# Performance work log

Measured on AMD Instinct MI355X. Metric: run time of the kernel, lower is better.

The kernel has to match this reference:

```python
import jax, jax.numpy as jnp
import numpy as np
from itertools import combinations, product

NQ = 10
DIM = 2 ** NQ
DEPTH = 1
ENC_PAIRS = [(q, q + 1) for q in range(0, NQ - 1, 2)] + [(q, q + 1) for q in range(1, NQ - 1, 2)]  # brick layer: even then odd
PYR = [(i, i + 1) for layer in range(NQ - 1) for i in range(NQ - layer - 1)]  # pyramid RBS wire pairs (45)
OBS_PAIRS = list(combinations(range(NQ), 2))  # 45 pairwise 2-local observables

_P = {'I': np.eye(2, dtype=np.complex128),
      'X': np.array([[0, 1], [1, 0]], dtype=np.complex128),
      'Y': np.array([[0, -1j], [1j, 0]], dtype=np.complex128),
      'Z': np.array([[1, 0], [0, -1]], dtype=np.complex128)}
_WORDS = [''.join(w) for w in product('IXYZ', repeat=2)][1:]  # PennyLane pauli_basis order, identity excluded
P15 = jnp.asarray(np.stack([np.kron(_P[w[0]], _P[w[1]]) for w in _WORDS]).astype(np.complex64))
XXm = jnp.asarray(np.kron(_P['X'], _P['X']).astype(np.complex64))
YYm = jnp.asarray(np.kron(_P['Y'], _P['Y']).astype(np.complex64))
ZZm = jnp.asarray(np.kron(_P['Z'], _P['Z']).astype(np.complex64))
I4 = jnp.eye(4, dtype=jnp.complex64)
_TRIL_I, _TRIL_J = np.tril_indices(4, -1)  # order matches create_Hermitian's count+j indexing


def _u3(t, p, l):
    c = jnp.cos(t / 2).astype(jnp.complex64)
    s = jnp.sin(t / 2).astype(jnp.complex64)
    return jnp.stack([jnp.stack([c, -jnp.exp(1j * l) * s]),
                      jnp.stack([jnp.exp(1j * p) * s, jnp.exp(1j * (p + l)) * c])])


def _ising(phi, P):
    # exp(-i*phi/2 * P) for P in {XX, YY, ZZ} (P^2 = I)
    return jnp.cos(phi / 2) * I4 - 1j * jnp.sin(phi / 2) * P


def _apply1(psi, U, w):
    # psi: (B, 2, ..., 2); single-qubit gate U (2,2) on wire w
    psi = jnp.moveaxis(psi, 1 + w, -1)
    sh = psi.shape
    out = jnp.einsum('ij,brj->bri', U, psi.reshape(sh[0], -1, 2)).reshape(sh)
    return jnp.moveaxis(out, -1, 1 + w)


def _apply2(psi, U, a, b):
    # two-qubit gate on wires (a,b), a is most-significant (PennyLane wire order). U: (4,4) or batched (B,4,4)
    psi = jnp.moveaxis(psi, (1 + a, 1 + b), (-2, -1))
    sh = psi.shape
    flat = psi.reshape(sh[0], -1, 4)
    eq = 'bij,brj->bri' if U.ndim == 3 else 'ij,brj->bri'
    out = jnp.einsum(eq, U, flat).reshape(sh)
    return jnp.moveaxis(out, (-2, -1), (1 + a, 1 + b))


def _build_H(A, B, D):
    # create_Hermitian: lower triangle A+iB, diag[0:3] = D[1:4], diag[3]=0, then h + h^dagger
    n = A.shape[0]
    h = jnp.zeros((n, 4, 4), jnp.complex64)
    h = h.at[:, _TRIL_I, _TRIL_J].set(A.astype(jnp.complex64) + 1j * B.astype(jnp.complex64))
    d = np.arange(3)
    h = h.at[:, d, d].set(D[:, 1:4].astype(jnp.complex64))
    return h + jnp.conj(jnp.swapaxes(h, -1, -2))


def setup_inputs() -> dict:
    key = jax.random.key(0)
    ks = jax.random.split(key, 9)
    f32 = jnp.float32
    return {
        'x': jax.random.normal(ks[0], (256, 512), f32),
        'W1': jax.random.normal(ks[1], (512, 256), f32) * (512 ** -0.5),
        'b1': jnp.zeros((256,), f32),
        'W2': jax.random.normal(ks[2], (256, 135), f32) * (256 ** -0.5),
        'b2': jnp.zeros((135,), f32),
        'qvit_params': 0.01 * jax.random.normal(ks[3], (DEPTH, len(PYR), 12), f32),
        'A': 2.0 * jax.random.normal(ks[4], (len(OBS_PAIRS), 6), f32),
        'B': 2.0 * jax.random.normal(ks[5], (len(OBS_PAIRS), 6), f32),
        'D': 2.0 * jax.random.normal(ks[6], (len(OBS_PAIRS), 4), f32),
    }


def reference(x, W1, b1, W2, b2, qvit_params, A, B, D):
    Bsz = x.shape[0]
    # enc_proj: Linear -> SiLU -> Linear
    enc = jax.nn.silu(x @ W1 + b1) @ W2 + b2  # (B, 135)
    # Brick-layer SpecialUnitary encoding: U = exp(i * sum theta_m P_m) via eigh
    theta = enc.reshape(Bsz, len(ENC_PAIRS), 15).astype(jnp.complex64)
    Hg = jnp.einsum('bgm,mij->bgij', theta, P15)  # Hermitian generators (B, 9, 4, 4)
    ew, V = jnp.linalg.eigh(Hg)
    Ue = jnp.einsum('bgik,bgk,bgjk->bgij', V, jnp.exp(1j * ew.astype(jnp.complex64)), jnp.conj(V))
    # |0...0>
    psi = jnp.zeros((Bsz, DIM), jnp.complex64).at[:, 0].set(1.0).reshape((Bsz,) + (2,) * NQ)
    for g, (a, b) in enumerate(ENC_PAIRS):
        psi = _apply2(psi, Ue[:, g], a, b)
    # QViT pyramid ansatz
    for ly in range(DEPTH):
        for g, (a, b) in enumerate(PYR):
            p = qvit_params[ly, g]
            psi = _apply1(psi, _u3(p[0], p[1], p[2]), a)
            psi = _apply2(psi, _ising(p[3], XXm), a, b)
            psi = _apply2(psi, _ising(p[4], YYm), a, b)
            psi = _apply2(psi, _ising(p[5], ZZm), a, b)
            psi = _apply1(psi, _u3(p[6], p[7], p[8]), a)
            psi = _apply2(psi, _ising(p[9], XXm), a, b)
            psi = _apply2(psi, _ising(p[10], YYm), a, b)
            psi = _apply2(psi, _ising(p[11], ZZm), a, b)
    # Pairwise ANO Hermitian expectations
    Hobs = _build_H(A, B, D)  # (45, 4, 4)
    outs = []
    for w, (a, b) in enumerate(OBS_PAIRS):
        pm = jnp.moveaxis(psi, (1 + a, 1 + b), (1, 2)).reshape(Bsz, 4, -1)
        outs.append(jnp.real(jnp.einsum('bir,ij,bjr->b', jnp.conj(pm), Hobs[w], pm)))
    return jnp.stack(outs, axis=1).astype(jnp.float32)
```

## Files before the change

### kernel.cpp

```cpp
#include <hip/hip_runtime.h>
#include <math.h>

#define NOBS 45
typedef float2 c32;

__device__ __constant__ int PA_s[NOBS] = {
    1,1,1,1,1,1,1,1,1, 0,0,0,0,0,0,0,0, 7,7,7,7,7,7,7, 6,6,6,6,6,6,
    5,5,5,5,5, 3,3,3,3, 2,2,2, 4,4, 9};
__device__ __constant__ int PB_s[NOBS] = {
    0,7,6,5,3,2,4,9,8, 7,6,5,3,2,4,9,8, 6,5,3,2,4,9,8, 5,3,2,4,9,8,
    3,2,4,9,8, 2,4,9,8, 4,9,8, 9,8, 8};
constexpr int TIc[6] = {1, 2, 2, 3, 3, 3};
constexpr int TJc[6] = {0, 0, 1, 0, 1, 2};

__device__ __forceinline__ c32 cfma(c32 a, c32 b, c32 c) {
    c.x = fmaf(a.x, b.x, fmaf(-a.y, b.y, c.x));
    c.y = fmaf(a.x, b.y, fmaf(a.y, b.x, c.y));
    return c;
}
__device__ __forceinline__ c32 cmul(c32 a, c32 b) {
    return make_float2(a.x * b.x - a.y * b.y, a.x * b.y + a.y * b.x);
}

template <int CTRL>
__device__ __forceinline__ float dppf(float x) {
    return __uint_as_float((unsigned)__builtin_amdgcn_update_dpp(
        0, (int)__float_as_uint(x), CTRL, 0xF, 0xF, true));
}
__device__ __forceinline__ float swap32f(float a) {
    auto r = __builtin_amdgcn_permlane32_swap(__float_as_uint(a), __float_as_uint(a), false, false);
    return (__uint_as_float(r[0]) + __uint_as_float(r[1])) - a;
}
#if __has_builtin(__builtin_amdgcn_permlane16_swap)
__device__ __forceinline__ float swap16f(float a) {
    auto r = __builtin_amdgcn_permlane16_swap(__float_as_uint(a), __float_as_uint(a), false, false);
    return (__uint_as_float(r[0]) + __uint_as_float(r[1])) - a;
}
#else
__device__ __forceinline__ float swap16f(float a) { return __shfl_xor(a, 16, 64); }
#endif
__device__ __forceinline__ float swz4f(float a) {
    return __uint_as_float(__builtin_amdgcn_ds_swizzle(__float_as_uint(a), 0x101F));
}
template <int M>
__device__ __forceinline__ float exf(float x) {
    float r = x;
    if constexpr ((M & 3) == 1) r = dppf<0xB1>(r);
    else if constexpr ((M & 3) == 2) r = dppf<0x4E>(r);
    else if constexpr ((M & 3) == 3) r = dppf<0x1B>(r);
    if constexpr (M & 4)  r = swz4f(r);
    if constexpr (M & 8)  r = dppf<0x128>(r);
    if constexpr (M & 16) r = swap16f(r);
    if constexpr (M & 32) r = swap32f(r);
    return r;
}
template <int M>
__device__ __forceinline__ c32 exch(c32 a) { return make_float2(exf<M>(a.x), exf<M>(a.y)); }
__device__ __forceinline__ c32 swap32c(c32 a) { return make_float2(swap32f(a.x), swap32f(a.y)); }

__device__ __forceinline__ float wave_reduce63(float x) {
    x += dppf<0x111>(x);
    x += dppf<0x112>(x);
    x += dppf<0x114>(x);
    x += dppf<0x118>(x);
    x += dppf<0x142>(x);
    x += dppf<0x143>(x);
    return x;
}

__device__ __forceinline__ int insert2(int t, int pl, int ph) {
    int low  = t & ((1 << pl) - 1);
    int rest = t >> pl;
    int nm   = ph - 1 - pl;
    int mid  = rest & ((1 << nm) - 1);
    int high = rest >> nm;
    return low | (mid << (pl + 1)) | (high << (ph + 1));
}

template <int W>
__device__ __forceinline__ c32 pE(int r, int c) {
    if constexpr (W == 0) return make_float2((r == c) ? 1.f : 0.f, 0.f);
    else if constexpr (W == 1) return make_float2((r != c) ? 1.f : 0.f, 0.f);
    else if constexpr (W == 2) return make_float2(0.f, (r == c) ? 0.f : ((r == 0) ? -1.f : 1.f));
    else return make_float2((r == c) ? ((r == 0) ? 1.f : -1.f) : 0.f, 0.f);
}
template <int W0, int W1>
__device__ __forceinline__ void paccum(c32& H, float th, int i1, int i2, int j1, int j2) {
    c32 a = pE<W0>(i1, j1), b = pE<W1>(i2, j2);
    c32 p = cmul(a, b);
    H.x = fmaf(th, p.x, H.x);
    H.y = fmaf(th, p.y, H.y);
}

struct F16 { c32 u[16]; };
struct FLoc { c32 a[4]; c32 b[4]; };
struct F4 { c32 uS, uB, uA, uC; };

__device__ __forceinline__ F16 loadF16(const c32* __restrict__ U) {
    F16 f;
#pragma unroll
    for (int i = 0; i < 16; i++) f.u[i] = U[i];
    return f;
}
__device__ __forceinline__ FLoc loadLoc(const c32* __restrict__ U, int ln) {
    int bb = (ln >> 5) & 1;
    const c32* U0 = U + bb * 4;
    const c32* U1 = U + (2 | bb) * 4;
    int c00 = bb, c01 = 2 | bb, c10 = bb ^ 1, c11 = 2 | (bb ^ 1);
    FLoc f;
    f.a[0] = U0[c00]; f.a[1] = U0[c01]; f.a[2] = U0[c10]; f.a[3] = U0[c11];
    f.b[0] = U1[c00]; f.b[1] = U1[c01]; f.b[2] = U1[c10]; f.b[3] = U1[c11];
    return f;
}
template <int QA, int QB>
__device__ __forceinline__ F4 loadL2(const c32* __restrict__ U, int ln) {
    int bA = (ln >> QA) & 1, bB = (ln >> QB) & 1;
    int r = (bA << 1) | bB;
    const c32* Ur = U + r * 4;
    F4 f;
    f.uS = Ur[r]; f.uB = Ur[r ^ 1]; f.uA = Ur[r ^ 2]; f.uC = Ur[r ^ 3];
    return f;
}

__device__ __forceinline__ void applyLL(c32 v[4], const F16& f) {
    c32 n0 = cfma(f.u[0],  v[0], cfma(f.u[1],  v[1], cfma(f.u[2],  v[2], cmul(f.u[3],  v[3]))));
    c32 n1 = cfma(f.u[4],  v[0], cfma(f.u[5],  v[1], cfma(f.u[6],  v[2], cmul(f.u[7],  v[3]))));
    c32 n2 = cfma(f.u[8],  v[0], cfma(f.u[9],  v[1], cfma(f.u[10], v[2], cmul(f.u[11], v[3]))));
    c32 n3 = cfma(f.u[12], v[0], cfma(f.u[13], v[1], cfma(f.u[14], v[2], cmul(f.u[15], v[3]))));
    v[0] = n0; v[1] = n1; v[2] = n2; v[3] = n3;
}
__device__ __forceinline__ void applyLoc(c32 v[4], const FLoc& f) {
    c32 p0 = swap32c(v[0]), p1 = swap32c(v[1]), p2 = swap32c(v[2]), p3 = swap32c(v[3]);
    c32 n0 = cfma(f.a[0], v[0], cfma(f.a[1], v[1], cfma(f.a[2], p0, cmul(f.a[3], p1))));
    c32 n1 = cfma(f.b[0], v[0], cfma(f.b[1], v[1], cfma(f.b[2], p0, cmul(f.b[3], p1))));
    c32 n2 = cfma(f.a[0], v[2], cfma(f.a[1], v[3], cfma(f.a[2], p2, cmul(f.a[3], p3))));
    c32 n3 = cfma(f.b[0], v[2], cfma(f.b[1], v[3], cfma(f.b[2], p2, cmul(f.b[3], p3))));
    v[0] = n0; v[1] = n1; v[2] = n2; v[3] = n3;
}
template <int QA, int QB>
__device__ __forceinline__ void applyL2(c32 v[4], const F4& f) {
#pragma unroll
    for (int lc = 0; lc < 4; lc++) {
        c32 pB = exch<(1 << QB)>(v[lc]);
        c32 pA = exch<(1 << QA)>(v[lc]);
        c32 pC = exch<(1 << QA)>(pB);
        v[lc] = cfma(f.uS, v[lc], cfma(f.uB, pB, cfma(f.uA, pA, cmul(f.uC, pC))));
    }
}

__device__ __forceinline__ void dumpV(const c32 v[4], c32* __restrict__ psi, int t) {
#pragma unroll
    for (int lc = 0; lc < 4; lc++) psi[(t << 2) | lc] = v[lc];
}
__device__ __forceinline__ void loadV(c32 v[4], const c32* __restrict__ psi, int t) {
#pragma unroll
    for (int lc = 0; lc < 4; lc++) v[lc] = psi[(t << 2) | lc];
}
template <int PA, int PB>
__device__ __forceinline__ void ldsApply(const F16& f, c32* __restrict__ psi, int t) {
    constexpr int PL = (PA < PB) ? PA : PB, PH = (PA < PB) ? PB : PA;
    int base = insert2(t, PL, PH);
    constexpr int oa = 1 << PA, ob = 1 << PB;
    c32 g0 = psi[base], g1 = psi[base + ob], g2 = psi[base + oa], g3 = psi[base + oa + ob];
    c32 n0 = cfma(f.u[0],  g0, cfma(f.u[1],  g1, cfma(f.u[2],  g2, cmul(f.u[3],  g3))));
    c32 n1 = cfma(f.u[4],  g0, cfma(f.u[5],  g1, cfma(f.u[6],  g2, cmul(f.u[7],  g3))));
    c32 n2 = cfma(f.u[8],  g0, cfma(f.u[9],  g1, cfma(f.u[10], g2, cmul(f.u[11], g3))));
    c32 n3 = cfma(f.u[12], g0, cfma(f.u[13], g1, cfma(f.u[14], g2, cmul(f.u[15], g3))));
    psi[base] = n0; psi[base + ob] = n1; psi[base + oa] = n2; psi[base + oa + ob] = n3;
}

__global__ __launch_bounds__(256, 1) void mega_kernel(
    const float* __restrict__ x,  const float* __restrict__ W1, const float* __restrict__ b1,
    const float* __restrict__ W2, const float* __restrict__ b2, const float* __restrict__ qp,
    const float* __restrict__ Am, const float* __restrict__ Bm, const float* __restrict__ Dm,
    float* __restrict__ out) {
    __shared__ __align__(16) c32 psiS[1024];
    __shared__ c32 UeS[144];
    __shared__ c32 GpS[720];
    __shared__ float HbS[720];
    __shared__ float encS[136];
    __shared__ float redS[180];

    const int b = blockIdx.x, t = threadIdx.x, ln = t & 63;
    float* F = (float*)psiS;

    if (t < 128) ((float4*)F)[t] = ((const float4*)(x + (size_t)b * 512))[t];
    __syncthreads();
    {
        int q = t & 63, sl = t >> 6;
        float4 a4 = make_float4(0.f, 0.f, 0.f, 0.f);
#pragma unroll 16
        for (int kk = 0; kk < 128; kk++) {
            int k = sl * 128 + kk;
            float xk = F[k];
            const float4 w = *(const float4*)(W1 + (size_t)k * 256 + q * 4);
            a4.x = fmaf(xk, w.x, a4.x); a4.y = fmaf(xk, w.y, a4.y);
            a4.z = fmaf(xk, w.z, a4.z); a4.w = fmaf(xk, w.w, a4.w);
        }
        *(float4*)(F + 512 + sl * 256 + q * 4) = a4;
    }
    __syncthreads();
    {
        float hv = b1[t] + F[512 + t] + F[768 + t] + F[1024 + t] + F[1280 + t];
        hv = hv / (1.f + __expf(-hv));
        F[1536 + t] = hv;
    }
    __syncthreads();
    if (t < 135) {
        float a2 = b2[t], a3 = 0.f;
#pragma unroll 16
        for (int k = 0; k < 128; k++) {
            a2 = fmaf(F[1536 + k],       W2[(size_t)k * 135 + t],         a2);
            a3 = fmaf(F[1536 + 128 + k], W2[(size_t)(128 + k) * 135 + t], a3);
        }
        encS[t] = a2 + a3;
    }
    __syncthreads();

    c32* Mm = psiS;
    c32* Rb = psiS + 144;
    c32* TA = psiS + 288;
    if (t < 144) {
        int m = t >> 4, e = t & 15, i = e >> 2, j = e & 3;
        int i1 = i >> 1, i2 = i & 1, j1 = j >> 1, j2 = j & 1;
        const float* th = encS + m * 15;
        c32 H = make_float2(0.f, 0.f);
        paccum<0,1>(H, th[0],  i1,i2,j1,j2); paccum<0,2>(H, th[1],  i1,i2,j1,j2);
        paccum<0,3>(H, th[2],  i1,i2,j1,j2); paccum<1,0>(H, th[3],  i1,i2,j1,j2);
        paccum<1,1>(H, th[4],  i1,i2,j1,j2); paccum<1,2>(H, th[5],  i1,i2,j1,j2);
        paccum<1,3>(H, th[6],  i1,i2,j1,j2); paccum<2,0>(H, th[7],  i1,i2,j1,j2);
        paccum<2,1>(H, th[8],  i1,i2,j1,j2); paccum<2,2>(H, th[9],  i1,i2,j1,j2);
        paccum<2,3>(H, th[10], i1,i2,j1,j2); paccum<3,0>(H, th[11], i1,i2,j1,j2);
        paccum<3,1>(H, th[12], i1,i2,j1,j2); paccum<3,2>(H, th[13], i1,i2,j1,j2);
        paccum<3,3>(H, th[14], i1,i2,j1,j2);
        const float sc = 1.f / 64.f;
        Mm[t] = make_float2(-H.y * sc, H.x * sc);
        Rb[t] = make_float2((i == j) ? 1.f : 0.f, 0.f);
    } else if (t >= 234) {
        for (int w = t - 234; w < NOBS; w += 22) {
            float* Hf = HbS + w * 16;
            Hf[0] = 2.f * Dm[w * 4 + 1];
            Hf[1] = 2.f * Dm[w * 4 + 2];
            Hf[2] = 2.f * Dm[w * 4 + 3];
            Hf[3] = 0.f;
#pragma unroll
            for (int k = 0; k < 6; k++) {
                Hf[4 + 2 * k] = 2.f * Am[w * 6 + k];
                Hf[5 + 2 * k] = 2.f * Bm[w * 6 + k];
            }
        }
    }
    __syncthreads();
    c32 Mrow[4];
    if (t < 144) {
        int m = t >> 4, i = (t & 15) >> 2;
#pragma unroll
        for (int k = 0; k < 4; k++) Mrow[k] = Mm[m * 16 + i * 4 + k];
    }
#pragma unroll 1
    for (int step = 0; step < 13; step++) {
        if (t < 144) {
            int m = t >> 4, e = t & 15, i = e >> 2, j = e & 3;
            const c32* cur = (step & 1) ? UeS : Rb;
            c32 acc = make_float2(0.f, 0.f);
            c32 outv;
            if (step < 7) {
#pragma unroll
                for (int k = 0; k < 4; k++) acc = cfma(Mrow[k], cur[m * 16 + k * 4 + j], acc);
                float inv = 1.f / (float)(7 - step);
                outv = make_float2(fmaf(acc.x, inv, (i == j) ? 1.f : 0.f), acc.y * inv);
            } else {
#pragma unroll
                for (int k = 0; k < 4; k++)
                    acc = cfma(cur[m * 16 + i * 4 + k], cur[m * 16 + k * 4 + j], acc);
                outv = acc;
            }
            ((step & 1) ? Rb : UeS)[t] = outv;
        } else if (t >= 144 && t < 234 && step < 8) {
            int pt = t - 144, g = pt >> 1, ih = (pt & 1) << 1;
            const float* p = qp + g * 12;
            const c32* src = ((step & 1) ? TA : GpS) + g * 16;
            c32* dst = ((step & 1) ? GpS : TA) + g * 16;
#pragma unroll
            for (int r2 = 0; r2 < 2; r2++) {
                int i = ih + r2, i1 = i >> 1, i2 = i & 1;
                c32 row[4];
                if (step == 0) {
                    float s, c; __sincosf(p[0] * 0.5f, &s, &c);
                    c32 u0, u1;
                    if (i1 == 0) { u0 = make_float2(c, 0.f);
                                   u1 = make_float2(-__cosf(p[2]) * s, -__sinf(p[2]) * s); }
                    else { u0 = make_float2(__cosf(p[1]) * s, __sinf(p[1]) * s);
                           u1 = make_float2(__cosf(p[1] + p[2]) * c, __sinf(p[1] + p[2]) * c); }
#pragma unroll
                    for (int jj = 0; jj < 4; jj++) row[jj] = make_float2(0.f, 0.f);
                    row[i2] = u0; row[2 | i2] = u1;
                } else {
                    c32 coef0, coef1; int c0, c1;
                    if (step == 1 || step == 5) {
                        float s, c; __sincosf(p[step == 1 ? 3 : 9] * 0.5f, &s, &c);
                        c0 = i; coef0 = make_float2(c, 0.f);
                        c1 = i ^ 3; coef1 = make_float2(0.f, -s);
                    } else if (step == 2 || step == 6) {
                        float s, c; __sincosf(p[step == 2 ? 4 : 10] * 0.5f, &s, &c);
                        float yy = (i == 0 || i == 3) ? 1.f : -1.f;
                        c0 = i; coef0 = make_float2(c, 0.f);
                        c1 = i ^ 3; coef1 = make_float2(0.f, s * yy);
                    } else if (step == 3 || step == 7) {
                        float s, c; __sincosf(p[step == 3 ? 5 : 11] * 0.5f, &s, &c);
                        float zz = (i == 0 || i == 3) ? 1.f : -1.f;
                        c0 = i; coef0 = make_float2(c, -s * zz);
                        c1 = i; coef1 = make_float2(0.f, 0.f);
                    } else {
                        float s, c; __sincosf(p[6] * 0.5f, &s, &c);
                        if (i1 == 0) { coef0 = make_float2(c, 0.f);
                                       coef1 = make_float2(-__cosf(p[8]) * s, -__sinf(p[8]) * s); }
                        else { coef0 = make_float2(__cosf(p[7]) * s, __sinf(p[7]) * s);
                               coef1 = make_float2(__cosf(p[7] + p[8]) * c, __sinf(p[7] + p[8]) * c); }
                        c0 = i2; c1 = 2 | i2;
                    }
#pragma unroll
                    for (int jj = 0; jj < 4; jj++)
                        row[jj] = cfma(coef0, src[c0 * 4 + jj], cmul(coef1, src[c1 * 4 + jj]));
                }
#pragma unroll
                for (int jj = 0; jj < 4; jj++) dst[i * 4 + jj] = row[jj];
            }
        }
        __syncthreads();
    }

    c32 v[4];
#pragma unroll
    for (int lc = 0; lc < 4; lc++) v[lc] = make_float2(0.f, 0.f);
    if (t == 0) v[0] = make_float2(1.f, 0.f);

    applyLL(v, loadF16(UeS + 0));
    applyL2<5, 4>(v, loadL2<5, 4>(UeS + 16, ln));
    applyL2<3, 1>(v, loadL2<3, 1>(UeS + 32, ln));
    applyL2<0, 2>(v, loadL2<0, 2>(UeS + 48, ln));
    dumpV(v, psiS, t); __syncthreads();
    ldsApply<9, 8>(loadF16(UeS + 64), psiS, t); __syncthreads();
    loadV(v, psiS, t);
    applyLoc(v, loadLoc(UeS + 80, ln));
    applyL2<4, 3>(v, loadL2<4, 3>(UeS + 96, ln));
    applyL2<1, 0>(v, loadL2<1, 0>(UeS + 112, ln));
    dumpV(v, psiS, t); __syncthreads();
    ldsApply<4, 9>(loadF16(UeS + 128), psiS, t); __syncthreads();
    loadV(v, psiS, t);

    {
        int g = 0;
#pragma unroll 1
        for (int layer = 0; layer < 9; layer++) {
            const int amax = 8 - layer;
            applyLL(v, loadF16(GpS + (g++) * 16));
            if (amax >= 1) applyLoc(v, loadLoc(GpS + (g++) * 16, ln));
            if (amax >= 2) applyL2<5, 4>(v, loadL2<5, 4>(GpS + (g++) * 16, ln));
            if (amax >= 3) applyL2<4, 3>(v, loadL2<4, 3>(GpS + (g++) * 16, ln));
            if (amax >= 4) applyL2<3, 1>(v, loadL2<3, 1>(GpS + (g++) * 16, ln));
            if (amax >= 5) applyL2<1, 0>(v, loadL2<1, 0>(GpS + (g++) * 16, ln));
            if (amax >= 6) applyL2<0, 2>(v, loadL2<0, 2>(GpS + (g++) * 16, ln));
            if (amax >= 7) {
                dumpV(v, psiS, t); __syncthreads();
                ldsApply<4, 9>(loadF16(GpS + (g++) * 16), psiS, t); __syncthreads();
                if (amax >= 8) {
                    ldsApply<9, 8>(loadF16(GpS + (g++) * 16), psiS, t); __syncthreads();
                }
                loadV(v, psiS, t);
            }
        }
    }

    dumpV(v, psiS, t);
    __syncthreads();
#pragma unroll 1
    for (int w0 = 0; w0 < NOBS; w0 += 5) {
        float pr[5];
#pragma unroll
        for (int u = 0; u < 5; u++) {
            const int w = w0 + u;
            const int pa = PA_s[w], pb = PB_s[w];
            const int pl = (pa < pb) ? pa : pb, phh = (pa < pb) ? pb : pa;
            const int oa = 1 << pa, ob = 1 << pb;
            int i0 = insert2(t, pl, phh);
            c32 vg[4];
            vg[0] = psiS[i0];      vg[1] = psiS[i0 + ob];
            vg[2] = psiS[i0 + oa]; vg[3] = psiS[i0 + oa + ob];
            const float* Hf = HbS + w * 16;
            float r = Hf[0] * fmaf(vg[0].x, vg[0].x, vg[0].y * vg[0].y)
                    + Hf[1] * fmaf(vg[1].x, vg[1].x, vg[1].y * vg[1].y)
                    + Hf[2] * fmaf(vg[2].x, vg[2].x, vg[2].y * vg[2].y);
#pragma unroll
            for (int k = 0; k < 6; k++) {
                c32 vi = vg[TIc[k]], vj = vg[TJc[k]];
                float cx = fmaf(vi.x, vj.x, vi.y * vj.y);
                float cy = fmaf(vi.x, vj.y, -vi.y * vj.x);
                r = fmaf(Hf[4 + 2 * k], cx, r);
                r = fmaf(-Hf[5 + 2 * k], cy, r);
            }
            pr[u] = wave_reduce63(r);
        }
        if (ln == 63) {
#pragma unroll
            for (int u = 0; u < 5; u++) redS[(w0 + u) * 4 + (t >> 6)] = pr[u];
        }
    }
    __syncthreads();
    if (t < NOBS)
        out[(size_t)b * NOBS + t] = redS[t * 4] + redS[t * 4 + 1] + redS[t * 4 + 2] + redS[t * 4 + 3];
}

extern "C" void kernel_launch(void* const* d_in, const int* in_sizes, int n_in,
                              void* d_out, int out_size, void* d_ws, size_t ws_size,
                              hipStream_t stream) {
    (void)in_sizes; (void)n_in; (void)out_size; (void)d_ws; (void)ws_size;
    const float* x  = (const float*)d_in[0];
    const float* W1 = (const float*)d_in[1];
    const float* b1 = (const float*)d_in[2];
    const float* W2 = (const float*)d_in[3];
    const float* b2 = (const float*)d_in[4];
    const float* qp = (const float*)d_in[5];
    const float* Am = (const float*)d_in[6];
    const float* Bm = (const float*)d_in[7];
    const float* Dm = (const float*)d_in[8];
    float* out = (float*)d_out;

    hipLaunchKernelGGL(mega_kernel, dim3(256), dim3(256), 0, stream,
                       x, W1, b1, W2, b2, qp, Am, Bm, Dm, out);
}
```

Before: 112.2 us.

## Double threads per block and remap qubits to halve per-thread state

Doubles the block to 512 threads, so each thread holds 2 amplitudes instead of 4. The qubit-to-bit mapping becomes natural order: one qubit sits in the register index, low qubits in the lane, and qubits 6-9 go through shared memory. Shared-memory gates now use ping-pong buffers, with each thread computing two output rows. The encoder MLP, the observable reduction and the gate loops are repartitioned across 8 waves, and the loops are fully unrolled. The aim is more wave-level parallelism and shorter per-thread dependency chains. The cost is more barriers and cross-lane exchanges, plus each 4x4 gate row being loaded separately per half-block.

```diff
diff --git a/kernel.cpp b/kernel.cpp
--- a/kernel.cpp
+++ b/kernel.cpp
@@ -4,14 +4,12 @@
 #define NOBS 45
 typedef float2 c32;
 
-__device__ __constant__ int PA_s[NOBS] = {
-    1,1,1,1,1,1,1,1,1, 0,0,0,0,0,0,0,0, 7,7,7,7,7,7,7, 6,6,6,6,6,6,
-    5,5,5,5,5, 3,3,3,3, 2,2,2, 4,4, 9};
-__device__ __constant__ int PB_s[NOBS] = {
-    0,7,6,5,3,2,4,9,8, 7,6,5,3,2,4,9,8, 6,5,3,2,4,9,8, 5,3,2,4,9,8,
-    3,2,4,9,8, 2,4,9,8, 4,9,8, 9,8, 8};
-constexpr int TIc[6] = {1, 2, 2, 3, 3, 3};
-constexpr int TJc[6] = {0, 0, 1, 0, 1, 2};
+constexpr int OAc[NOBS] = {
+    0,0,0,0,0,0,0,0,0, 1,1,1,1,1,1,1,1, 2,2,2,2,2,2,2, 3,3,3,3,3,3,
+    4,4,4,4,4, 5,5,5,5, 6,6,6, 7,7, 8};
+constexpr int OBc[NOBS] = {
+    1,2,3,4,5,6,7,8,9, 2,3,4,5,6,7,8,9, 3,4,5,6,7,8,9, 4,5,6,7,8,9,
+    5,6,7,8,9, 6,7,8,9, 7,8,9, 8,9, 9};
 
 __device__ __forceinline__ c32 cfma(c32 a, c32 b, c32 c) {
     c.x = fmaf(a.x, b.x, fmaf(-a.y, b.y, c.x));
@@ -56,7 +54,6 @@
 }
 template <int M>
 __device__ __forceinline__ c32 exch(c32 a) { return make_float2(exf<M>(a.x), exf<M>(a.y)); }
-__device__ __forceinline__ c32 swap32c(c32 a) { return make_float2(swap32f(a.x), swap32f(a.y)); }
 
 __device__ __forceinline__ float wave_reduce63(float x) {
     x += dppf<0x111>(x);
@@ -92,25 +89,34 @@
     H.y = fmaf(th, p.y, H.y);
 }
 
-struct F16 { c32 u[16]; };
+struct F8v { c32 u[8]; };
 struct FLoc { c32 a[4]; c32 b[4]; };
 struct F4 { c32 uS, uB, uA, uC; };
 
-__device__ __forceinline__ F16 loadF16(const c32* __restrict__ U) {
-    F16 f;
-#pragma unroll
-    for (int i = 0; i < 16; i++) f.u[i] = U[i];
+__device__ __forceinline__ F8v loadF8(const c32* __restrict__ U, int rr) {
+    F8v f;
+    const c32* R = U + (rr << 3);
+#pragma unroll
+    for (int i = 0; i < 8; i++) f.u[i] = R[i];
     return f;
 }
-__device__ __forceinline__ FLoc loadLoc(const c32* __restrict__ U, int ln) {
-    int bb = (ln >> 5) & 1;
-    const c32* U0 = U + bb * 4;
-    const c32* U1 = U + (2 | bb) * 4;
-    int c00 = bb, c01 = 2 | bb, c10 = bb ^ 1, c11 = 2 | (bb ^ 1);
+template <int LB>
+__device__ __forceinline__ FLoc loadLocLane(const c32* __restrict__ U, int ln) {
+    int lb = (ln >> LB) & 1;
+    const c32* R0 = U + lb * 4;
+    const c32* R1 = U + (2 | lb) * 4;
     FLoc f;
-    f.a[0] = U0[c00]; f.a[1] = U0[c01]; f.a[2] = U0[c10]; f.a[3] = U0[c11];
-    f.b[0] = U1[c00]; f.b[1] = U1[c01]; f.b[2] = U1[c10]; f.b[3] = U1[c11];
+    f.a[0] = R0[lb]; f.a[1] = R0[lb ^ 1]; f.a[2] = R0[2 | lb]; f.a[3] = R0[2 | (lb ^ 1)];
+    f.b[0] = R1[lb]; f.b[1] = R1[lb ^ 1]; f.b[2] = R1[2 | lb]; f.b[3] = R1[2 | (lb ^ 1)];
     return f;
+}
+template <int LB>
+__device__ __forceinline__ void applyLocLane(c32 v[2], const FLoc& f) {
+    c32 p0 = exch<(1 << LB)>(v[0]);
+    c32 p1 = exch<(1 << LB)>(v[1]);
+    c32 n0 = cfma(f.a[3], p1, cfma(f.a[2], v[1], cfma(f.a[1], p0, cmul(f.a[0], v[0]))));
+    c32 n1 = cfma(f.b[3], p1, cfma(f.b[2], v[1], cfma(f.b[1], p0, cmul(f.b[0], v[0]))));
+    v[0] = n0; v[1] = n1;
 }
 template <int QA, int QB>
 __device__ __forceinline__ F4 loadL2(const c32* __restrict__ U, int ln) {
@@ -121,68 +127,55 @@
     f.uS = Ur[r]; f.uB = Ur[r ^ 1]; f.uA = Ur[r ^ 2]; f.uC = Ur[r ^ 3];
     return f;
 }
-
-__device__ __forceinline__ void applyLL(c32 v[4], const F16& f) {
-    c32 n0 = cfma(f.u[0],  v[0], cfma(f.u[1],  v[1], cfma(f.u[2],  v[2], cmul(f.u[3],  v[3]))));
-    c32 n1 = cfma(f.u[4],  v[0], cfma(f.u[5],  v[1], cfma(f.u[6],  v[2], cmul(f.u[7],  v[3]))));
-    c32 n2 = cfma(f.u[8],  v[0], cfma(f.u[9],  v[1], cfma(f.u[10], v[2], cmul(f.u[11], v[3]))));
-    c32 n3 = cfma(f.u[12], v[0], cfma(f.u[13], v[1], cfma(f.u[14], v[2], cmul(f.u[15], v[3]))));
-    v[0] = n0; v[1] = n1; v[2] = n2; v[3] = n3;
-}
-__device__ __forceinline__ void applyLoc(c32 v[4], const FLoc& f) {
-    c32 p0 = swap32c(v[0]), p1 = swap32c(v[1]), p2 = swap32c(v[2]), p3 = swap32c(v[3]);
-    c32 n0 = cfma(f.a[0], v[0], cfma(f.a[1], v[1], cfma(f.a[2], p0, cmul(f.a[3], p1))));
-    c32 n1 = cfma(f.b[0], v[0], cfma(f.b[1], v[1], cfma(f.b[2], p0, cmul(f.b[3], p1))));
-    c32 n2 = cfma(f.a[0], v[2], cfma(f.a[1], v[3], cfma(f.a[2], p2, cmul(f.a[3], p3))));
-    c32 n3 = cfma(f.b[0], v[2], cfma(f.b[1], v[3], cfma(f.b[2], p2, cmul(f.b[3], p3))));
-    v[0] = n0; v[1] = n1; v[2] = n2; v[3] = n3;
-}
 template <int QA, int QB>
-__device__ __forceinline__ void applyL2(c32 v[4], const F4& f) {
-#pragma unroll
-    for (int lc = 0; lc < 4; lc++) {
-        c32 pB = exch<(1 << QB)>(v[lc]);
-        c32 pA = exch<(1 << QA)>(v[lc]);
-        c32 pC = exch<(1 << QA)>(pB);
-        v[lc] = cfma(f.uS, v[lc], cfma(f.uB, pB, cfma(f.uA, pA, cmul(f.uC, pC))));
-    }
-}
-
-__device__ __forceinline__ void dumpV(const c32 v[4], c32* __restrict__ psi, int t) {
-#pragma unroll
-    for (int lc = 0; lc < 4; lc++) psi[(t << 2) | lc] = v[lc];
-}
-__device__ __forceinline__ void loadV(c32 v[4], const c32* __restrict__ psi, int t) {
-#pragma unroll
-    for (int lc = 0; lc < 4; lc++) v[lc] = psi[(t << 2) | lc];
+__device__ __forceinline__ void applyL2(c32 v[2], const F4& f) {
+    c32 pB[2], pA[2], pC[2];
+#pragma unroll
+    for (int lc = 0; lc < 2; lc++) pB[lc] = exch<(1 << QB)>(v[lc]);
+#pragma unroll
+    for (int lc = 0; lc < 2; lc++) pA[lc] = exch<(1 << QA)>(v[lc]);
+#pragma unroll
+    for (int lc = 0; lc < 2; lc++) pC[lc] = exch<(1 << QA)>(pB[lc]);
+#pragma unroll
+    for (int lc = 0; lc < 2; lc++)
+        v[lc] = cfma(f.uC, pC[lc], cfma(f.uA, pA[lc], cfma(f.uB, pB[lc], cmul(f.uS, v[lc]))));
+}
+
+__device__ __forceinline__ void dumpV2(const c32 v[2], c32* __restrict__ psi, int t) {
+    psi[t * 2] = v[0]; psi[t * 2 + 1] = v[1];
+}
+__device__ __forceinline__ void loadV2(c32 v[2], const c32* __restrict__ psi, int t) {
+    v[0] = psi[t * 2]; v[1] = psi[t * 2 + 1];
 }
 template <int PA, int PB>
-__device__ __forceinline__ void ldsApply(const F16& f, c32* __restrict__ psi, int t) {
-    constexpr int PL = (PA < PB) ? PA : PB, PH = (PA < PB) ? PB : PA;
-    int base = insert2(t, PL, PH);
+__device__ __forceinline__ void ldsApply2(const F8v& f, const c32* __restrict__ src,
+                                          c32* __restrict__ dst, int g, int rr) {
+    int base = insert2(g, PA, PB);
     constexpr int oa = 1 << PA, ob = 1 << PB;
-    c32 g0 = psi[base], g1 = psi[base + ob], g2 = psi[base + oa], g3 = psi[base + oa + ob];
-    c32 n0 = cfma(f.u[0],  g0, cfma(f.u[1],  g1, cfma(f.u[2],  g2, cmul(f.u[3],  g3))));
-    c32 n1 = cfma(f.u[4],  g0, cfma(f.u[5],  g1, cfma(f.u[6],  g2, cmul(f.u[7],  g3))));
-    c32 n2 = cfma(f.u[8],  g0, cfma(f.u[9],  g1, cfma(f.u[10], g2, cmul(f.u[11], g3))));
-    c32 n3 = cfma(f.u[12], g0, cfma(f.u[13], g1, cfma(f.u[14], g2, cmul(f.u[15], g3))));
-    psi[base] = n0; psi[base + ob] = n1; psi[base + oa] = n2; psi[base + oa + ob] = n3;
-}
-
-__global__ __launch_bounds__(256, 1) void mega_kernel(
+    c32 g0 = src[base], g1 = src[base + ob], g2 = src[base + oa], g3 = src[base + oa + ob];
+    c32 n0 = cfma(f.u[3], g3, cfma(f.u[2], g2, cfma(f.u[1], g1, cmul(f.u[0], g0))));
+    c32 n1 = cfma(f.u[7], g3, cfma(f.u[6], g2, cfma(f.u[5], g1, cmul(f.u[4], g0))));
+    dst[base + rr * oa] = n0;
+    dst[base + rr * oa + ob] = n1;
+}
+
+__global__ __launch_bounds__(512, 1) void mega_kernel(
     const float* __restrict__ x,  const float* __restrict__ W1, const float* __restrict__ b1,
     const float* __restrict__ W2, const float* __restrict__ b2, const float* __restrict__ qp,
     const float* __restrict__ Am, const float* __restrict__ Bm, const float* __restrict__ Dm,
     float* __restrict__ out) {
-    __shared__ __align__(16) c32 psiS[1024];
+    __shared__ __align__(16) c32 psiS[2048];
     __shared__ c32 UeS[144];
     __shared__ c32 GpS[720];
     __shared__ float HbS[720];
-    __shared__ float encS[136];
-    __shared__ float redS[180];
+    __shared__ float encS0[136], encS1[136];
+    __shared__ float redS[NOBS * 8];
 
     const int b = blockIdx.x, t = threadIdx.x, ln = t & 63;
+    const int gg = t & 255, rr = t >> 8, wv = t >> 6;
     float* F = (float*)psiS;
+    c32* psiA = psiS;
+    c32* psiB = psiS + 1024;
 
     if (t < 128) ((float4*)F)[t] = ((const float4*)(x + (size_t)b * 512))[t];
     __syncthreads();
@@ -190,8 +183,8 @@
         int q = t & 63, sl = t >> 6;
         float4 a4 = make_float4(0.f, 0.f, 0.f, 0.f);
 #pragma unroll 16
-        for (int kk = 0; kk < 128; kk++) {
-            int k = sl * 128 + kk;
+        for (int kk = 0; kk < 64; kk++) {
+            int k = sl * 64 + kk;
             float xk = F[k];
             const float4 w = *(const float4*)(W1 + (size_t)k * 256 + q * 4);
             a4.x = fmaf(xk, w.x, a4.x); a4.y = fmaf(xk, w.y, a4.y);
@@ -200,20 +193,31 @@
         *(float4*)(F + 512 + sl * 256 + q * 4) = a4;
     }
     __syncthreads();
-    {
-        float hv = b1[t] + F[512 + t] + F[768 + t] + F[1024 + t] + F[1280 + t];
+    if (t < 256) {
+        float hv = b1[t];
+#pragma unroll
+        for (int s = 0; s < 8; s++) hv += F[512 + s * 256 + t];
         hv = hv / (1.f + __expf(-hv));
-        F[1536 + t] = hv;
+        F[2560 + t] = hv;
     }
     __syncthreads();
     if (t < 135) {
-        float a2 = b2[t], a3 = 0.f;
+        float a0 = b2[t], a1 = 0.f;
 #pragma unroll 16
-        for (int k = 0; k < 128; k++) {
-            a2 = fmaf(F[1536 + k],       W2[(size_t)k * 135 + t],         a2);
-            a3 = fmaf(F[1536 + 128 + k], W2[(size_t)(128 + k) * 135 + t], a3);
-        }
-        encS[t] = a2 + a3;
+        for (int k = 0; k < 64; k++) {
+            a0 = fmaf(F[2560 + k],      W2[(size_t)k * 135 + t],        a0);
+            a1 = fmaf(F[2560 + 64 + k], W2[(size_t)(64 + k) * 135 + t], a1);
+        }
+        encS0[t] = a0 + a1;
+    } else if (t >= 256 && t < 391) {
+        int c = t - 256;
+        float a0 = 0.f, a1 = 0.f;
+#pragma unroll 16
+        for (int k = 0; k < 64; k++) {
+            a0 = fmaf(F[2560 + 128 + k], W2[(size_t)(128 + k) * 135 + c], a0);
+            a1 = fmaf(F[2560 + 192 + k], W2[(size_t)(192 + k) * 135 + c], a1);
+        }
+        encS1[c] = a0 + a1;
     }
     __syncthreads();
 
@@ -223,31 +227,32 @@
     if (t < 144) {
         int m = t >> 4, e = t & 15, i = e >> 2, j = e & 3;
         int i1 = i >> 1, i2 = i & 1, j1 = j >> 1, j2 = j & 1;
-        const float* th = encS + m * 15;
+        const int o = m * 15;
         c32 H = make_float2(0.f, 0.f);
-        paccum<0,1>(H, th[0],  i1,i2,j1,j2); paccum<0,2>(H, th[1],  i1,i2,j1,j2);
-        paccum<0,3>(H, th[2],  i1,i2,j1,j2); paccum<1,0>(H, th[3],  i1,i2,j1,j2);
-        paccum<1,1>(H, th[4],  i1,i2,j1,j2); paccum<1,2>(H, th[5],  i1,i2,j1,j2);
-        paccum<1,3>(H, th[6],  i1,i2,j1,j2); paccum<2,0>(H, th[7],  i1,i2,j1,j2);
-        paccum<2,1>(H, th[8],  i1,i2,j1,j2); paccum<2,2>(H, th[9],  i1,i2,j1,j2);
-        paccum<2,3>(H, th[10], i1,i2,j1,j2); paccum<3,0>(H, th[11], i1,i2,j1,j2);
-        paccum<3,1>(H, th[12], i1,i2,j1,j2); paccum<3,2>(H, th[13], i1,i2,j1,j2);
-        paccum<3,3>(H, th[14], i1,i2,j1,j2);
+#define TH(J) (encS0[o + (J)] + encS1[o + (J)])
+        paccum<0,1>(H, TH(0),  i1,i2,j1,j2); paccum<0,2>(H, TH(1),  i1,i2,j1,j2);
+        paccum<0,3>(H, TH(2),  i1,i2,j1,j2); paccum<1,0>(H, TH(3),  i1,i2,j1,j2);
+        paccum<1,1>(H, TH(4),  i1,i2,j1,j2); paccum<1,2>(H, TH(5),  i1,i2,j1,j2);
+        paccum<1,3>(H, TH(6),  i1,i2,j1,j2); paccum<2,0>(H, TH(7),  i1,i2,j1,j2);
+        paccum<2,1>(H, TH(8),  i1,i2,j1,j2); paccum<2,2>(H, TH(9),  i1,i2,j1,j2);
+        paccum<2,3>(H, TH(10), i1,i2,j1,j2); paccum<3,0>(H, TH(11), i1,i2,j1,j2);
+        paccum<3,1>(H, TH(12), i1,i2,j1,j2); paccum<3,2>(H, TH(13), i1,i2,j1,j2);
+        paccum<3,3>(H, TH(14), i1,i2,j1,j2);
+#undef TH
         const float sc = 1.f / 64.f;
         Mm[t] = make_float2(-H.y * sc, H.x * sc);
         Rb[t] = make_float2((i == j) ? 1.f : 0.f, 0.f);
-    } else if (t >= 234) {
-        for (int w = t - 234; w < NOBS; w += 22) {
-            float* Hf = HbS + w * 16;
-            Hf[0] = 2.f * Dm[w * 4 + 1];
-            Hf[1] = 2.f * Dm[w * 4 + 2];
-            Hf[2] = 2.f * Dm[w * 4 + 3];
-            Hf[3] = 0.f;
-#pragma unroll
-            for (int k = 0; k < 6; k++) {
-                Hf[4 + 2 * k] = 2.f * Am[w * 6 + k];
-                Hf[5 + 2 * k] = 2.f * Bm[w * 6 + k];
-            }
+    } else if (t >= 384 && t < 384 + NOBS) {
+        const int w = t - 384;
+        float* Hf = HbS + w * 16;
+        Hf[0] = 2.f * Dm[w * 4 + 1];
+        Hf[1] = 2.f * Dm[w * 4 + 2];
+        Hf[2] = 2.f * Dm[w * 4 + 3];
+        Hf[3] = 0.f;
+#pragma unroll
+        for (int k = 0; k < 6; k++) {
+            Hf[4 + 2 * k] = 2.f * Am[w * 6 + k];
+            Hf[5 + 2 * k] = 2.f * Bm[w * 6 + k];
         }
     }
     __syncthreads();
@@ -284,7 +289,7 @@
 #pragma unroll
             for (int r2 = 0; r2 < 2; r2++) {
                 int i = ih + r2, i1 = i >> 1, i2 = i & 1;
-                c32 row[4];
+                c32 rowv[4];
                 if (step == 0) {
                     float s, c; __sincosf(p[0] * 0.5f, &s, &c);
                     c32 u0, u1;
@@ -293,8 +298,8 @@
                     else { u0 = make_float2(__cosf(p[1]) * s, __sinf(p[1]) * s);
                            u1 = make_float2(__cosf(p[1] + p[2]) * c, __sinf(p[1] + p[2]) * c); }
 #pragma unroll
-                    for (int jj = 0; jj < 4; jj++) row[jj] = make_float2(0.f, 0.f);
-                    row[i2] = u0; row[2 | i2] = u1;
+                    for (int jj = 0; jj < 4; jj++) rowv[jj] = make_float2(0.f, 0.f);
+                    rowv[i2] = u0; rowv[2 | i2] = u1;
                 } else {
                     c32 coef0, coef1; int c0, c1;
                     if (step == 1 || step == 5) {
@@ -321,94 +326,118 @@
                     }
 #pragma unroll
                     for (int jj = 0; jj < 4; jj++)
-                        row[jj] = cfma(coef0, src[c0 * 4 + jj], cmul(coef1, src[c1 * 4 + jj]));
+                        rowv[jj] = cfma(coef0, src[c0 * 4 + jj], cmul(coef1, src[c1 * 4 + jj]));
                 }
 #pragma unroll
-                for (int jj = 0; jj < 4; jj++) dst[i * 4 + jj] = row[jj];
+                for (int jj = 0; jj < 4; jj++) dst[i * 4 + jj] = rowv[jj];
             }
         }
         __syncthreads();
     }
 
-    c32 v[4];
-#pragma unroll
-    for (int lc = 0; lc < 4; lc++) v[lc] = make_float2(0.f, 0.f);
+    c32 v[2];
+    v[0] = make_float2(0.f, 0.f);
+    v[1] = make_float2(0.f, 0.f);
     if (t == 0) v[0] = make_float2(1.f, 0.f);
 
-    applyLL(v, loadF16(UeS + 0));
-    applyL2<5, 4>(v, loadL2<5, 4>(UeS + 16, ln));
-    applyL2<3, 1>(v, loadL2<3, 1>(UeS + 32, ln));
-    applyL2<0, 2>(v, loadL2<0, 2>(UeS + 48, ln));
-    dumpV(v, psiS, t); __syncthreads();
-    ldsApply<9, 8>(loadF16(UeS + 64), psiS, t); __syncthreads();
-    loadV(v, psiS, t);
-    applyLoc(v, loadLoc(UeS + 80, ln));
-    applyL2<4, 3>(v, loadL2<4, 3>(UeS + 96, ln));
-    applyL2<1, 0>(v, loadL2<1, 0>(UeS + 112, ln));
-    dumpV(v, psiS, t); __syncthreads();
-    ldsApply<4, 9>(loadF16(UeS + 128), psiS, t); __syncthreads();
-    loadV(v, psiS, t);
+    applyLocLane<0>(v, loadLocLane<0>(UeS + 0, ln));
+    applyL2<1, 2>(v, loadL2<1, 2>(UeS + 16, ln));
+    applyL2<3, 4>(v, loadL2<3, 4>(UeS + 32, ln));
+    applyL2<0, 1>(v, loadL2<0, 1>(UeS + 80, ln));
+    applyL2<2, 3>(v, loadL2<2, 3>(UeS + 96, ln));
+    dumpV2(v, psiA, t); __syncthreads();
+    ldsApply2<6, 7>(loadF8(UeS + 48, rr), psiA, psiB, gg, rr); __syncthreads();
+    ldsApply2<8, 9>(loadF8(UeS + 64, rr), psiB, psiA, gg, rr); __syncthreads();
+    loadV2(v, psiA, t);
+    applyL2<4, 5>(v, loadL2<4, 5>(UeS + 112, ln));
+    dumpV2(v, psiA, t); __syncthreads();
+    ldsApply2<7, 8>(loadF8(UeS + 128, rr), psiA, psiB, gg, rr); __syncthreads();
+    loadV2(v, psiB, t);
 
     {
         int g = 0;
-#pragma unroll 1
+#pragma unroll
         for (int layer = 0; layer < 9; layer++) {
             const int amax = 8 - layer;
-            applyLL(v, loadF16(GpS + (g++) * 16));
-            if (amax >= 1) applyLoc(v, loadLoc(GpS + (g++) * 16, ln));
-            if (amax >= 2) applyL2<5, 4>(v, loadL2<5, 4>(GpS + (g++) * 16, ln));
-            if (amax >= 3) applyL2<4, 3>(v, loadL2<4, 3>(GpS + (g++) * 16, ln));
-            if (amax >= 4) applyL2<3, 1>(v, loadL2<3, 1>(GpS + (g++) * 16, ln));
-            if (amax >= 5) applyL2<1, 0>(v, loadL2<1, 0>(GpS + (g++) * 16, ln));
-            if (amax >= 6) applyL2<0, 2>(v, loadL2<0, 2>(GpS + (g++) * 16, ln));
-            if (amax >= 7) {
-                dumpV(v, psiS, t); __syncthreads();
-                ldsApply<4, 9>(loadF16(GpS + (g++) * 16), psiS, t); __syncthreads();
-                if (amax >= 8) {
-                    ldsApply<9, 8>(loadF16(GpS + (g++) * 16), psiS, t); __syncthreads();
+            applyLocLane<0>(v, loadLocLane<0>(GpS + (g++) * 16, ln));
+            if (amax >= 1) applyL2<0, 1>(v, loadL2<0, 1>(GpS + (g++) * 16, ln));
+            if (amax >= 2) applyL2<1, 2>(v, loadL2<1, 2>(GpS + (g++) * 16, ln));
+            if (amax >= 3) applyL2<2, 3>(v, loadL2<2, 3>(GpS + (g++) * 16, ln));
+            if (amax >= 4) applyL2<3, 4>(v, loadL2<3, 4>(GpS + (g++) * 16, ln));
+            if (amax >= 5) applyL2<4, 5>(v, loadL2<4, 5>(GpS + (g++) * 16, ln));
+            if (amax >= 6) {
+                dumpV2(v, psiA, t); __syncthreads();
+                ldsApply2<6, 7>(loadF8(GpS + (g++) * 16, rr), psiA, psiB, gg, rr);
+                __syncthreads();
+                if (amax >= 7) {
+                    ldsApply2<7, 8>(loadF8(GpS + (g++) * 16, rr), psiB, psiA, gg, rr);
+                    __syncthreads();
+                    if (amax >= 8) {
+                        ldsApply2<8, 9>(loadF8(GpS + (g++) * 16, rr), psiA, psiB, gg, rr);
+                        __syncthreads();
+                        loadV2(v, psiB, t);
+                    } else {
+                        loadV2(v, psiA, t);
+                    }
+                } else {
+                    loadV2(v, psiB, t);
                 }
-                loadV(v, psiS, t);
             }
         }
     }
 
-    dumpV(v, psiS, t);
-    __syncthreads();
-#pragma unroll 1
+    dumpV2(v, psiA, t);
+    __syncthreads();
+#pragma unroll
     for (int w0 = 0; w0 < NOBS; w0 += 5) {
         float pr[5];
 #pragma unroll
         for (int u = 0; u < 5; u++) {
             const int w = w0 + u;
-            const int pa = PA_s[w], pb = PB_s[w];
-            const int pl = (pa < pb) ? pa : pb, phh = (pa < pb) ? pb : pa;
+            const int pa = OAc[w], pb = OBc[w];
             const int oa = 1 << pa, ob = 1 << pb;
-            int i0 = insert2(t, pl, phh);
-            c32 vg[4];
-            vg[0] = psiS[i0];      vg[1] = psiS[i0 + ob];
-            vg[2] = psiS[i0 + oa]; vg[3] = psiS[i0 + oa + ob];
+            int i0 = insert2(gg, pa, pb);
             const float* Hf = HbS + w * 16;
-            float r = Hf[0] * fmaf(vg[0].x, vg[0].x, vg[0].y * vg[0].y)
-                    + Hf[1] * fmaf(vg[1].x, vg[1].x, vg[1].y * vg[1].y)
-                    + Hf[2] * fmaf(vg[2].x, vg[2].x, vg[2].y * vg[2].y);
-#pragma unroll
-            for (int k = 0; k < 6; k++) {
-                c32 vi = vg[TIc[k]], vj = vg[TJc[k]];
-                float cx = fmaf(vi.x, vj.x, vi.y * vj.y);
-                float cy = fmaf(vi.x, vj.y, -vi.y * vj.x);
-                r = fmaf(Hf[4 + 2 * k], cx, r);
-                r = fmaf(-Hf[5 + 2 * k], cy, r);
+            c32 g0 = psiA[i0], g1 = psiA[i0 + ob], g2 = psiA[i0 + oa], g3 = psiA[i0 + oa + ob];
+            float r;
+            if (rr == 0) {
+                r = Hf[0] * fmaf(g0.x, g0.x, g0.y * g0.y)
+                  + Hf[1] * fmaf(g1.x, g1.x, g1.y * g1.y)
+                  + Hf[2] * fmaf(g2.x, g2.x, g2.y * g2.y);
+                float cx0 = fmaf(g1.x, g0.x, g1.y * g0.y);
+                float cy0 = fmaf(g1.x, g0.y, -g1.y * g0.x);
+                r = fmaf(Hf[4], cx0, r); r = fmaf(-Hf[5], cy0, r);
+                float cx1 = fmaf(g2.x, g0.x, g2.y * g0.y);
+                float cy1 = fmaf(g2.x, g0.y, -g2.y * g0.x);
+                r = fmaf(Hf[6], cx1, r); r = fmaf(-Hf[7], cy1, r);
+            } else {
+                float cx0 = fmaf(g2.x, g1.x, g2.y * g1.y);
+                float cy0 = fmaf(g2.x, g1.y, -g2.y * g1.x);
+                r = Hf[8] * cx0 - Hf[9] * cy0;
+                float cx1 = fmaf(g3.x, g0.x, g3.y * g0.y);
+                float cy1 = fmaf(g3.x, g0.y, -g3.y * g0.x);
+                r = fmaf(Hf[10], cx1, r); r = fmaf(-Hf[11], cy1, r);
+                float cx2 = fmaf(g3.x, g1.x, g3.y * g1.y);
+                float cy2 = fmaf(g3.x, g1.y, -g3.y * g1.x);
+                r = fmaf(Hf[12], cx2, r); r = fmaf(-Hf[13], cy2, r);
+                float cx3 = fmaf(g3.x, g2.x, g3.y * g2.y);
+                float cy3 = fmaf(g3.x, g2.y, -g3.y * g2.x);
+                r = fmaf(Hf[14], cx3, r); r = fmaf(-Hf[15], cy3, r);
             }
             pr[u] = wave_reduce63(r);
         }
         if (ln == 63) {
 #pragma unroll
-            for (int u = 0; u < 5; u++) redS[(w0 + u) * 4 + (t >> 6)] = pr[u];
-        }
-    }
-    __syncthreads();
-    if (t < NOBS)
-        out[(size_t)b * NOBS + t] = redS[t * 4] + redS[t * 4 + 1] + redS[t * 4 + 2] + redS[t * 4 + 3];
+            for (int u = 0; u < 5; u++) redS[(w0 + u) * 8 + wv] = pr[u];
+        }
+    }
+    __syncthreads();
+    if (t < NOBS) {
+        float s = 0.f;
+#pragma unroll
+        for (int k = 0; k < 8; k++) s += redS[t * 8 + k];
+        out[(size_t)b * NOBS + t] = s;
+    }
 }
 
 extern "C" void kernel_launch(void* const* d_in, const int* in_sizes, int n_in,
@@ -426,6 +455,6 @@
     const float* Dm = (const float*)d_in[8];
     float* out = (float*)d_out;
 
-    hipLaunchKernelGGL(mega_kernel, dim3(256), dim3(256), 0, stream,
+    hipLaunchKernelGGL(mega_kernel, dim3(256), dim3(512), 0, stream,
                        x, W1, b1, W2, b2, qp, Am, Bm, Dm, out);
 }
```

New measurement: 105.6 us. -6.0%, faster.
